# Kernel tuning notes

Hardware: AMD Instinct MI355X
Metric: run time of the kernel (lower is better)

## Reference

```python
import jax, jax.numpy as jnp
import numpy as np

H = 64
EPS = 1e-5


def _lstm_layer(x, w_ih, w_hh, b_ih, b_hh):
    """Single LSTM layer, batch_first input x: [B, T, I]. PyTorch gate order i,f,g,o."""
    B, T, _ = x.shape
    # precompute input contributions for all timesteps: [B, T, 4H]
    xw = jnp.einsum('bti,gi->btg', x, w_ih) + (b_ih + b_hh)
    xw = jnp.swapaxes(xw, 0, 1)  # [T, B, 4H] for scan over time

    def step(carry, xw_t):
        h, c = carry
        gates = xw_t + h @ w_hh.T  # [B, 4H]
        i, f, g, o = jnp.split(gates, 4, axis=-1)
        i = jax.nn.sigmoid(i)
        f = jax.nn.sigmoid(f)
        g = jnp.tanh(g)
        o = jax.nn.sigmoid(o)
        c = f * c + i * g
        h = o * jnp.tanh(c)
        return (h, c), h

    h0 = jnp.zeros((B, H), x.dtype)
    (_, _), hs = jax.lax.scan(step, (h0, h0), xw)
    return jnp.swapaxes(hs, 0, 1)  # [B, T, H]


def setup_inputs() -> dict:
    key = jax.random.key(0)
    ks = jax.random.split(key, 16)
    B, T, F = 4096, 256, 32
    s = 1.0 / np.sqrt(H)  # PyTorch LSTM init scale
    inp = {
        'x': jax.random.normal(ks[0], (B, T, F), jnp.float32),
        'w_ih0': jax.random.uniform(ks[1], (4 * H, F), jnp.float32, -s, s),
        'w_hh0': jax.random.uniform(ks[2], (4 * H, H), jnp.float32, -s, s),
        'b_ih0': jax.random.uniform(ks[3], (4 * H,), jnp.float32, -s, s),
        'b_hh0': jax.random.uniform(ks[4], (4 * H,), jnp.float32, -s, s),
        'w_ih1': jax.random.uniform(ks[5], (4 * H, H), jnp.float32, -s, s),
        'w_hh1': jax.random.uniform(ks[6], (4 * H, H), jnp.float32, -s, s),
        'b_ih1': jax.random.uniform(ks[7], (4 * H,), jnp.float32, -s, s),
        'b_hh1': jax.random.uniform(ks[8], (4 * H,), jnp.float32, -s, s),
        'ln_g': jnp.ones((H,), jnp.float32),
        'ln_b': jnp.zeros((H,), jnp.float32),
        'w1': jax.random.uniform(ks[9], (64, H), jnp.float32, -s, s),
        'b1': jax.random.uniform(ks[10], (64,), jnp.float32, -s, s),
        'w2': jax.random.uniform(ks[11], (1, 64), jnp.float32, -0.125, 0.125),
        'b2': jax.random.uniform(ks[12], (1,), jnp.float32, -0.125, 0.125),
    }
    return inp


def reference(x, w_ih0, w_hh0, b_ih0, b_hh0, w_ih1, w_hh1, b_ih1, b_hh1,
              ln_g, ln_b, w1, b1, w2, b2):
    out0 = _lstm_layer(x, w_ih0, w_hh0, b_ih0, b_hh0)      # [B, T, H]
    out1 = _lstm_layer(out0, w_ih1, w_hh1, b_ih1, b_hh1)   # [B, T, H]
    last = out1[:, -1, :]                                   # [B, H]
    # LayerNorm
    mu = jnp.mean(last, axis=-1, keepdims=True)
    var = jnp.mean(jnp.square(last - mu), axis=-1, keepdims=True)
    ln = (last - mu) * jax.lax.rsqrt(var + EPS) * ln_g + ln_b
    # MLP head
    h = jax.nn.relu(ln @ w1.T + b1)
    y = h @ w2.T + b2                                       # [B, 1]
    return y[:, 0]
```

## Files before the change

kernel.cpp:

```cpp
#include <hip/hip_runtime.h>

#define TSEQ 256
#define FIN  32
#define HID  64

typedef _Float16 f16x8 __attribute__((ext_vector_type(8)));
typedef float    f32x4 __attribute__((ext_vector_type(4)));

__device__ __forceinline__ float sigm(float x) {
    return __builtin_amdgcn_rcpf(1.0f + __expf(-x));
}
__device__ __forceinline__ float tanh_fast(float x) {
    float e = __expf(2.0f * x);
    return 1.0f - 2.0f * __builtin_amdgcn_rcpf(e + 1.0f);
}
__device__ __forceinline__ float wsum(float v) {
    #pragma unroll
    for (int off = 32; off > 0; off >>= 1) v += __shfl_xor(v, off, 64);
    return v;
}

__global__ __launch_bounds__(1024, 4)
void lstm_fused(const float* __restrict__ x,
                const float* __restrict__ w_ih0, const float* __restrict__ w_hh0,
                const float* __restrict__ b_ih0, const float* __restrict__ b_hh0,
                const float* __restrict__ w_ih1, const float* __restrict__ w_hh1,
                const float* __restrict__ b_ih1, const float* __restrict__ b_hh1,
                const float* __restrict__ ln_g, const float* __restrict__ ln_b,
                const float* __restrict__ w1, const float* __restrict__ b1,
                const float* __restrict__ w2, const float* __restrict__ b2,
                float* __restrict__ out)
{
    __shared__ __align__(16) _Float16 X[2][16][32];
    __shared__ __align__(16) _Float16 H0[2][16][72];
    __shared__ __align__(16) _Float16 H1[2][16][72];
    __shared__ __align__(16) float HF[16][68];
    __shared__ __align__(16) float LNB[16][64];

    const int tid  = threadIdx.x;
    const int wave = tid >> 6;
    const int lane = tid & 63;
    const int q    = lane >> 4;
    const int lm   = lane & 15;
    const int q8   = q * 8;
    const int b0   = blockIdx.x * 16;

    const int np   = wave * 16 + lm;
    const int drow = np >> 2;
    const int ty   = np & 3;
    const int row  = ty * 64 + drow;
    const int dq   = wave * 4 + q;

    f16x8 w0f[3], w1f[4];
    f32x4 bias0, bias1;
    {
        const float* p0 = w_ih0 + row * FIN + q8;
        const float* p1 = w_hh0 + row * HID + q8;
        const float* p2 = w_hh0 + row * HID + 32 + q8;
        const float* p3 = w_ih1 + row * HID + q8;
        const float* p4 = w_ih1 + row * HID + 32 + q8;
        const float* p5 = w_hh1 + row * HID + q8;
        const float* p6 = w_hh1 + row * HID + 32 + q8;
        #pragma unroll
        for (int j = 0; j < 8; ++j) {
            w0f[0][j] = (_Float16)p0[j];
            w0f[1][j] = (_Float16)p1[j];
            w0f[2][j] = (_Float16)p2[j];
            w1f[0][j] = (_Float16)p3[j];
            w1f[1][j] = (_Float16)p4[j];
            w1f[2][j] = (_Float16)p5[j];
            w1f[3][j] = (_Float16)p6[j];
        }
        #pragma unroll
        for (int r = 0; r < 4; ++r) {
            bias0[r] = b_ih0[r * 64 + dq] + b_hh0[r * 64 + dq];
            bias1[r] = b_ih1[r * 64 + dq] + b_hh1[r * 64 + dq];
        }
    }

    for (int i = tid; i < 2 * 16 * 72; i += 1024) {
        ((_Float16*)H0)[i] = (_Float16)0.0f;
        ((_Float16*)H1)[i] = (_Float16)0.0f;
    }
    const bool xthr = tid < 512;
    const int xrow = (tid >> 5) & 15, xcol = tid & 31;
    const float* xbase = x + (size_t)(b0 + xrow) * TSEQ * FIN + xcol;
    float xw = 0.0f;
    if (xthr) {
        X[0][xrow][xcol] = (_Float16)xbase[0];
        xw = xbase[FIN];
    }
    float c0 = 0.0f, c1 = 0.0f;
    __syncthreads();

    for (int i = 0; i <= TSEQ; ++i) {
        const int p = i & 1;

        float xnew = 0.0f;
        if (xthr && i + 2 < TSEQ) xnew = xbase[(size_t)(i + 2) * FIN];

        f16x8 rx   = *reinterpret_cast<const f16x8*>(&X[p][lm][q8]);
        f16x8 rh0a = *reinterpret_cast<const f16x8*>(&H0[p ^ 1][lm][q8]);
        f16x8 rh0b = *reinterpret_cast<const f16x8*>(&H0[p ^ 1][lm][32 + q8]);
        f16x8 rh1a = *reinterpret_cast<const f16x8*>(&H1[p][lm][q8]);
        f16x8 rh1b = *reinterpret_cast<const f16x8*>(&H1[p][lm][32 + q8]);

        f32x4 aA, aB;
        if (i < TSEQ) {
            aA = bias0;
            aA = __builtin_amdgcn_mfma_f32_16x16x32_f16(w0f[0], rx,   aA, 0, 0, 0);
            aA = __builtin_amdgcn_mfma_f32_16x16x32_f16(w0f[1], rh0a, aA, 0, 0, 0);
            aA = __builtin_amdgcn_mfma_f32_16x16x32_f16(w0f[2], rh0b, aA, 0, 0, 0);
        }
        if (i >= 1) {
            aB = bias1;
            aB = __builtin_amdgcn_mfma_f32_16x16x32_f16(w1f[0], rh0a, aB, 0, 0, 0);
            aB = __builtin_amdgcn_mfma_f32_16x16x32_f16(w1f[1], rh0b, aB, 0, 0, 0);
            aB = __builtin_amdgcn_mfma_f32_16x16x32_f16(w1f[2], rh1a, aB, 0, 0, 0);
            aB = __builtin_amdgcn_mfma_f32_16x16x32_f16(w1f[3], rh1b, aB, 0, 0, 0);
        }

        if (i < TSEQ) {
            float ig = sigm(aA[0]);
            float fg = sigm(aA[1]);
            float gg = tanh_fast(aA[2]);
            float og = sigm(aA[3]);
            c0 = fg * c0 + ig * gg;
            float h = og * tanh_fast(c0);
            H0[p][lm][dq] = (_Float16)h;
        }
        if (i >= 1) {
            float ig = sigm(aB[0]);
            float fg = sigm(aB[1]);
            float gg = tanh_fast(aB[2]);
            float og = sigm(aB[3]);
            c1 = fg * c1 + ig * gg;
            float h = og * tanh_fast(c1);
            H1[p ^ 1][lm][dq] = (_Float16)h;
            if (i == TSEQ) HF[lm][dq] = h;
        }
        if (xthr && i + 1 < TSEQ) X[p ^ 1][xrow][xcol] = (_Float16)xw;
        xw = xnew;
        __syncthreads();
    }

    const float lngv = ln_g[lane], lnbv = ln_b[lane];
    const float b1v = b1[lane], w2v = w2[lane];
    const float* w1row = w1 + lane * 64;
    {
        float v  = HF[wave][lane];
        float mu = wsum(v) * (1.0f / 64.0f);
        float dv = v - mu;
        float var = wsum(dv * dv) * (1.0f / 64.0f);
        float ln = dv * rsqrtf(var + 1e-5f) * lngv + lnbv;
        LNB[wave][lane] = ln;
        float s = b1v;
        #pragma unroll
        for (int dd = 0; dd < 64; ++dd)
            s = fmaf(LNB[wave][dd], w1row[dd], s);
        s = fmaxf(s, 0.0f);
        float y = wsum(s * w2v);
        if (lane == 0) out[b0 + wave] = y + b2[0];
    }
}

extern "C" void kernel_launch(void* const* d_in, const int* in_sizes, int n_in,
                              void* d_out, int out_size, void* d_ws, size_t ws_size,
                              hipStream_t stream) {
    const float* x     = (const float*)d_in[0];
    const float* w_ih0 = (const float*)d_in[1];
    const float* w_hh0 = (const float*)d_in[2];
    const float* b_ih0 = (const float*)d_in[3];
    const float* b_hh0 = (const float*)d_in[4];
    const float* w_ih1 = (const float*)d_in[5];
    const float* w_hh1 = (const float*)d_in[6];
    const float* b_ih1 = (const float*)d_in[7];
    const float* b_hh1 = (const float*)d_in[8];
    const float* ln_g  = (const float*)d_in[9];
    const float* ln_b  = (const float*)d_in[10];
    const float* w1    = (const float*)d_in[11];
    const float* b1    = (const float*)d_in[12];
    const float* w2    = (const float*)d_in[13];
    const float* b2    = (const float*)d_in[14];
    lstm_fused<<<dim3(256), dim3(1024), 0, stream>>>(
        x, w_ih0, w_hh0, b_ih0, b_hh0,
        w_ih1, w_hh1, b_ih1, b_hh1,
        ln_g, ln_b, w1, b1, w2, b2, (float*)d_out);
}
```

Measured before the change: 389.1 us.

## Fuse LSTM gate math, peel time loop, and spread x loads across waves

Merges the sigmoid and tanh calls of each LSTM cell into one function that shares reciprocals, computing i*g and o*tanh(c) with one rcp each and clamping c before the exp. It also peels the first and last timesteps and unrolls the loop by two so the parity and boundary branches become compile-time constants. The x prefetch now uses 32 lanes in every wave, one batch row per wave, rather than the first 512 threads. These changes are meant to cut transcendental work and per-step control overhead on the serial recurrence; fusing the reciprocals slightly changes numerics and risks overflow for large gate values.

```diff
diff --git a/kernel.cpp b/kernel.cpp
--- a/kernel.cpp
+++ b/kernel.cpp
@@ -7,17 +7,23 @@
 typedef _Float16 f16x8 __attribute__((ext_vector_type(8)));
 typedef float    f32x4 __attribute__((ext_vector_type(4)));
 
-__device__ __forceinline__ float sigm(float x) {
-    return __builtin_amdgcn_rcpf(1.0f + __expf(-x));
-}
-__device__ __forceinline__ float tanh_fast(float x) {
-    float e = __expf(2.0f * x);
-    return 1.0f - 2.0f * __builtin_amdgcn_rcpf(e + 1.0f);
-}
 __device__ __forceinline__ float wsum(float v) {
     #pragma unroll
     for (int off = 32; off > 0; off >>= 1) v += __shfl_xor(v, off, 64);
     return v;
+}
+
+__device__ __forceinline__ float lstm_cell(const f32x4 g, float& c) {
+    float ei = __expf(-g[0]);
+    float ef = __expf(-g[1]);
+    float yg = __expf(2.0f * g[2]);
+    float eo = __expf(-g[3]);
+    float sf = __builtin_amdgcn_rcpf(1.0f + ef);
+    float ig = (yg - 1.0f) * __builtin_amdgcn_rcpf((1.0f + ei) * (yg + 1.0f));
+    c = fmaf(sf, c, ig);
+    float cc = fminf(fmaxf(c, -15.0f), 15.0f);
+    float yc = __expf(2.0f * cc);
+    return (yc - 1.0f) * __builtin_amdgcn_rcpf((1.0f + eo) * (yc + 1.0f));
 }
 
 __global__ __launch_bounds__(1024, 4)
@@ -82,67 +88,66 @@
         ((_Float16*)H0)[i] = (_Float16)0.0f;
         ((_Float16*)H1)[i] = (_Float16)0.0f;
     }
-    const bool xthr = tid < 512;
-    const int xrow = (tid >> 5) & 15, xcol = tid & 31;
-    const float* xbase = x + (size_t)(b0 + xrow) * TSEQ * FIN + xcol;
-    float xw = 0.0f;
-    if (xthr) {
-        X[0][xrow][xcol] = (_Float16)xbase[0];
-        xw = xbase[FIN];
-    }
+    const bool xlane = lane < 32;
+    const int  xcol  = lane & 31;
+    const float* xbase = x + (size_t)(b0 + wave) * TSEQ * FIN + xcol;
+    if (xlane) X[0][wave][xcol] = (_Float16)xbase[0];
+    float xw = xbase[FIN];
+
     float c0 = 0.0f, c1 = 0.0f;
     __syncthreads();
 
-    for (int i = 0; i <= TSEQ; ++i) {
-        const int p = i & 1;
+#define INTERVAL(P, DO_A, DO_B, DO_XSTORE, DO_XLOAD, XI)                        \
+    {                                                                           \
+        float xnew = 0.0f;                                                      \
+        if (DO_XLOAD) xnew = xbase[(size_t)(XI) * FIN];                         \
+        f16x8 rh0a = *reinterpret_cast<const f16x8*>(&H0[(P) ^ 1][lm][q8]);     \
+        f16x8 rh0b = *reinterpret_cast<const f16x8*>(&H0[(P) ^ 1][lm][32 + q8]);\
+        if (DO_A) {                                                             \
+            f16x8 rx = *reinterpret_cast<const f16x8*>(&X[P][lm][q8]);          \
+            f32x4 aA = bias0;                                                   \
+            aA = __builtin_amdgcn_mfma_f32_16x16x32_f16(w0f[0], rx,   aA, 0, 0, 0); \
+            aA = __builtin_amdgcn_mfma_f32_16x16x32_f16(w0f[1], rh0a, aA, 0, 0, 0); \
+            aA = __builtin_amdgcn_mfma_f32_16x16x32_f16(w0f[2], rh0b, aA, 0, 0, 0); \
+            float hA = lstm_cell(aA, c0);                                       \
+            H0[P][lm][dq] = (_Float16)hA;                                       \
+        }                                                                       \
+        if (DO_B) {                                                             \
+            f16x8 rh1a = *reinterpret_cast<const f16x8*>(&H1[P][lm][q8]);       \
+            f16x8 rh1b = *reinterpret_cast<const f16x8*>(&H1[P][lm][32 + q8]);  \
+            f32x4 aB = bias1;                                                   \
+            aB = __builtin_amdgcn_mfma_f32_16x16x32_f16(w1f[0], rh0a, aB, 0, 0, 0); \
+            aB = __builtin_amdgcn_mfma_f32_16x16x32_f16(w1f[1], rh0b, aB, 0, 0, 0); \
+            aB = __builtin_amdgcn_mfma_f32_16x16x32_f16(w1f[2], rh1a, aB, 0, 0, 0); \
+            aB = __builtin_amdgcn_mfma_f32_16x16x32_f16(w1f[3], rh1b, aB, 0, 0, 0); \
+            float hB = lstm_cell(aB, c1);                                       \
+            H1[(P) ^ 1][lm][dq] = (_Float16)hB;                                 \
+            lastB = hB;                                                         \
+        }                                                                       \
+        if (DO_XSTORE && xlane) X[(P) ^ 1][wave][xcol] = (_Float16)xw;          \
+        xw = xnew;                                                              \
+        __syncthreads();                                                        \
+    }
 
-        float xnew = 0.0f;
-        if (xthr && i + 2 < TSEQ) xnew = xbase[(size_t)(i + 2) * FIN];
+    float lastB = 0.0f;
 
-        f16x8 rx   = *reinterpret_cast<const f16x8*>(&X[p][lm][q8]);
-        f16x8 rh0a = *reinterpret_cast<const f16x8*>(&H0[p ^ 1][lm][q8]);
-        f16x8 rh0b = *reinterpret_cast<const f16x8*>(&H0[p ^ 1][lm][32 + q8]);
-        f16x8 rh1a = *reinterpret_cast<const f16x8*>(&H1[p][lm][q8]);
-        f16x8 rh1b = *reinterpret_cast<const f16x8*>(&H1[p][lm][32 + q8]);
+    INTERVAL(0, true, false, true, true, 2)
 
-        f32x4 aA, aB;
-        if (i < TSEQ) {
-            aA = bias0;
-            aA = __builtin_amdgcn_mfma_f32_16x16x32_f16(w0f[0], rx,   aA, 0, 0, 0);
-            aA = __builtin_amdgcn_mfma_f32_16x16x32_f16(w0f[1], rh0a, aA, 0, 0, 0);
-            aA = __builtin_amdgcn_mfma_f32_16x16x32_f16(w0f[2], rh0b, aA, 0, 0, 0);
-        }
-        if (i >= 1) {
-            aB = bias1;
-            aB = __builtin_amdgcn_mfma_f32_16x16x32_f16(w1f[0], rh0a, aB, 0, 0, 0);
-            aB = __builtin_amdgcn_mfma_f32_16x16x32_f16(w1f[1], rh0b, aB, 0, 0, 0);
-            aB = __builtin_amdgcn_mfma_f32_16x16x32_f16(w1f[2], rh1a, aB, 0, 0, 0);
-            aB = __builtin_amdgcn_mfma_f32_16x16x32_f16(w1f[3], rh1b, aB, 0, 0, 0);
-        }
+    #pragma unroll 1
+    for (int ii = 0; ii < 127; ++ii) {
+        const int i1  = 2 * ii + 1;
+        const int xiA = (i1 + 2 > 255) ? 255 : i1 + 2;
+        const int xiB = (i1 + 3 > 255) ? 255 : i1 + 3;
+        INTERVAL(1, true, true, true, true, xiA)
+        INTERVAL(0, true, true, true, true, xiB)
+    }
 
-        if (i < TSEQ) {
-            float ig = sigm(aA[0]);
-            float fg = sigm(aA[1]);
-            float gg = tanh_fast(aA[2]);
-            float og = sigm(aA[3]);
-            c0 = fg * c0 + ig * gg;
-            float h = og * tanh_fast(c0);
-            H0[p][lm][dq] = (_Float16)h;
-        }
-        if (i >= 1) {
-            float ig = sigm(aB[0]);
-            float fg = sigm(aB[1]);
-            float gg = tanh_fast(aB[2]);
-            float og = sigm(aB[3]);
-            c1 = fg * c1 + ig * gg;
-            float h = og * tanh_fast(c1);
-            H1[p ^ 1][lm][dq] = (_Float16)h;
-            if (i == TSEQ) HF[lm][dq] = h;
-        }
-        if (xthr && i + 1 < TSEQ) X[p ^ 1][xrow][xcol] = (_Float16)xw;
-        xw = xnew;
-        __syncthreads();
-    }
+    INTERVAL(1, true, true, false, false, 0)
+    INTERVAL(0, false, true, false, false, 0)
+    HF[lm][dq] = lastB;
+    __syncthreads();
+
+#undef INTERVAL
 
     const float lngv = ln_g[lane], lnbv = ln_b[lane];
     const float b1v = b1[lane], w2v = w2[lane];
```

After: 370.5 us. 1.05x faster.
